# Kernel optimization log

Hardware: AMD Instinct MI355X
Metric: run time of the kernel (lower is better)

Reference implementation:

```python
import jax, jax.numpy as jnp
import numpy as np

B, S, D, E, NH, R, L = 512, 23, 768, 8, 8, 256, 50
TOP_K = 2
LN_EPS = 1e-5  # torch LayerNorm default


def _ln(x, g, b):
    m = jnp.mean(x, axis=-1, keepdims=True)
    v = jnp.mean((x - m) ** 2, axis=-1, keepdims=True)
    return (x - m) * jax.lax.rsqrt(v + LN_EPS) * g + b


def setup_inputs() -> dict:
    key = jax.random.key(0)
    it = iter(jax.random.split(key, 32))
    def p(shape, scale=0.02):
        return jax.random.normal(next(it), shape, dtype=jnp.float32) * scale
    inp = {
        'section_embeddings': jax.random.normal(next(it), (B, S, D), dtype=jnp.float32),
        'existing': jax.random.randint(next(it), (B, S), 0, 2, dtype=jnp.int32),
        'missing_table': p((S, D), 0.05),
        # DeepPositionEncoder per expert (num_layers=3): D->R->R->R->D + LN(D)
        'dpe_w0': p((E, D, R)), 'dpe_b0': jnp.zeros((E, R), jnp.float32),
        'dpe_w1': p((E, R, R)), 'dpe_b1': jnp.zeros((E, R), jnp.float32),
        'dpe_w2': p((E, R, R)), 'dpe_b2': jnp.zeros((E, R), jnp.float32),
        'dpe_wo': p((E, R, D)), 'dpe_bo': jnp.zeros((E, D), jnp.float32),
        'dpe_ln_g': jnp.ones((E, D), jnp.float32), 'dpe_ln_b': jnp.zeros((E, D), jnp.float32),
        # fusion_mlp: cat([context,pos]) (2D)->R->D ; W1 split into context/pos halves
        'fus_w1c': p((E, D, R)), 'fus_w1p': p((E, D, R)), 'fus_b1': jnp.zeros((E, R), jnp.float32),
        'fus_w2': p((E, R, D)), 'fus_b2': jnp.zeros((E, D), jnp.float32),
        # gate_mlp: 2D->R->1, sigmoid
        'gate_w1c': p((E, D, R)), 'gate_w1p': p((E, D, R)), 'gate_b1': jnp.zeros((E, R), jnp.float32),
        'gate_w2': p((E, R, 1)), 'gate_b2': jnp.zeros((E, 1), jnp.float32),
        'exp_ln_g': jnp.ones((E, D), jnp.float32), 'exp_ln_b': jnp.zeros((E, D), jnp.float32),
        # router: 2D->R->E
        'rtr_w1': p((2 * D, R)), 'rtr_b1': jnp.zeros((R,), jnp.float32),
        'rtr_w2': p((R, E)), 'rtr_b2': jnp.zeros((E,), jnp.float32),
        # SectionDimReducer: D->D//2->R + LN(R)
        'red_w1': p((D, D // 2)), 'red_b1': jnp.zeros((D // 2,), jnp.float32),
        'red_w2': p((D // 2, R)), 'red_b2': jnp.zeros((R,), jnp.float32),
        'red_ln_g': jnp.ones((R,), jnp.float32), 'red_ln_b': jnp.zeros((R,), jnp.float32),
        # MultiheadAttention (embed_dim=R, heads=NH)
        'qkv_w': p((3, R, R)), 'qkv_b': jnp.zeros((3, R), jnp.float32),
        'out_w': p((R, R)), 'out_b': jnp.zeros((R,), jnp.float32),
        # predictor
        'pred_w': p((R, L)), 'pred_b': jnp.zeros((L,), jnp.float32),
    }
    return inp


def reference(section_embeddings, existing, missing_table,
              dpe_w0, dpe_b0, dpe_w1, dpe_b1, dpe_w2, dpe_b2, dpe_wo, dpe_bo,
              dpe_ln_g, dpe_ln_b,
              fus_w1c, fus_w1p, fus_b1, fus_w2, fus_b2,
              gate_w1c, gate_w1p, gate_b1, gate_w2, gate_b2,
              exp_ln_g, exp_ln_b,
              rtr_w1, rtr_b1, rtr_w2, rtr_b2,
              red_w1, red_b1, red_w2, red_b2, red_ln_g, red_ln_b,
              qkv_w, qkv_b, out_w, out_b, pred_w, pred_b):
    mask = existing.astype(section_embeddings.dtype)[..., None]         # [B,S,1]
    # masked mean context over present sections
    context = (section_embeddings * mask).sum(1) / (mask.sum(1) + 1e-8)  # [B,D]
    T = B * S
    default = jnp.broadcast_to(missing_table[None], (B, S, D)).reshape(T, D)
    ctx = jnp.broadcast_to(context[:, None, :], (B, S, D)).reshape(T, D)
    # --- all experts, dense (as in source) ---
    h = jax.nn.relu(jnp.einsum('td,edh->teh', default, dpe_w0) + dpe_b0)
    h = jax.nn.relu(jnp.einsum('teh,ehk->tek', h, dpe_w1) + dpe_b1)
    h = jax.nn.relu(jnp.einsum('teh,ehk->tek', h, dpe_w2) + dpe_b2)
    pos = _ln(jnp.einsum('teh,ehd->ted', h, dpe_wo) + dpe_bo + default[:, None, :],
              dpe_ln_g, dpe_ln_b)                                        # [T,E,D]
    hf = jax.nn.relu(jnp.einsum('td,edh->teh', ctx, fus_w1c)
                     + jnp.einsum('ted,edh->teh', pos, fus_w1p) + fus_b1)
    cand = jnp.einsum('teh,ehd->ted', hf, fus_w2) + fus_b2
    hg = jax.nn.relu(jnp.einsum('td,edh->teh', ctx, gate_w1c)
                     + jnp.einsum('ted,edh->teh', pos, gate_w1p) + gate_b1)
    gate = jax.nn.sigmoid(jnp.einsum('teh,eho->teo', hg, gate_w2) + gate_b2)  # [T,E,1]
    exp_out = _ln(gate * cand + (1.0 - gate) * ctx[:, None, :], exp_ln_g, exp_ln_b)  # [T,E,D]
    # --- router: softmax -> top-k -> sparse scatter ---
    rin = jnp.concatenate([default, ctx], axis=-1)                      # [T,2D]
    scores = jax.nn.relu(rin @ rtr_w1 + rtr_b1) @ rtr_w2 + rtr_b2       # [T,E]
    w = jax.nn.softmax(scores, axis=-1)
    tv, ti = jax.lax.top_k(w, TOP_K)
    sw = jnp.zeros_like(w).at[jnp.arange(T)[:, None], ti].set(tv)       # [T,E]
    imputed = jnp.einsum('ted,te->td', exp_out, sw).reshape(B, S, D)
    sec = mask * section_embeddings + (1.0 - mask) * imputed            # [B,S,D]
    # --- reducer ---
    x = jax.nn.gelu(sec @ red_w1 + red_b1, approximate=False)
    x = jax.nn.gelu(x @ red_w2 + red_b2, approximate=False)
    x = _ln(x, red_ln_g, red_ln_b)                                      # [B,S,R]
    # --- MHA self-attention over sections ---
    hd = R // NH
    q = (x @ qkv_w[0] + qkv_b[0]).reshape(B, S, NH, hd)
    k = (x @ qkv_w[1] + qkv_b[1]).reshape(B, S, NH, hd)
    v = (x @ qkv_w[2] + qkv_b[2]).reshape(B, S, NH, hd)
    att = jax.nn.softmax(jnp.einsum('bqhd,bkhd->bhqk', q, k) / np.sqrt(hd), axis=-1)
    o = jnp.einsum('bhqk,bkhd->bqhd', att, v).reshape(B, S, R)
    o = o @ out_w + out_b
    logits = o.mean(axis=1) @ pred_w + pred_b                           # [B,L]
    return logits
```

## Files before the change

kernel.cpp:

```cpp
#include <hip/hip_runtime.h>
#include <hip/hip_bf16.h>
#include <math.h>

#define BB  512
#define SS  23
#define DD  768
#define EE  8
#define NHH 8
#define RR  256
#define HDD 32
#define LL  50
#define HH2 384
#define TT  (BB*SS)
#define LN_EPS 1e-5f
#define MAXWORK 1536
#define NCTX 4352
#define NACAP 12288

typedef short v8s __attribute__((ext_vector_type(8)));
typedef float v4f __attribute__((ext_vector_type(4)));

__device__ __forceinline__ float gelu(float v){
  return 0.5f*v*(1.f + erff(v*0.70710678118654752f));
}
__device__ __forceinline__ unsigned short f2b(float v){
  __hip_bfloat16 h = __float2bfloat16(v);
  return *reinterpret_cast<unsigned short*>(&h);
}

__device__ __forceinline__ float block_sum(float v, float* red, int nw){
  #pragma unroll
  for (int o = 32; o > 0; o >>= 1) v += __shfl_down(v, o, 64);
  int wid = threadIdx.x >> 6;
  __syncthreads();
  if ((threadIdx.x & 63) == 0) red[wid] = v;
  __syncthreads();
  float s = 0.f;
  for (int i = 0; i < nw; ++i) s += red[i];
  return s;
}

__global__ void k_context(const float* __restrict__ emb, const int* __restrict__ existing,
                          float* __restrict__ ctx, unsigned short* __restrict__ ctxbf){
  int b = blockIdx.x, tid = threadIdx.x;
  float acc0=0.f, acc1=0.f, acc2=0.f;
  int cnt = 0;
  for (int s = 0; s < SS; ++s){
    if (existing[b*SS + s]){
      ++cnt;
      const float* row = emb + ((size_t)(b*SS + s))*DD;
      acc0 += row[tid]; acc1 += row[tid+256]; acc2 += row[tid+512];
    }
  }
  float inv = 1.0f / ((float)cnt + 1e-8f);
  float v0 = acc0*inv, v1 = acc1*inv, v2 = acc2*inv;
  ctx[(size_t)b*DD + tid      ] = v0;
  ctx[(size_t)b*DD + tid + 256] = v1;
  ctx[(size_t)b*DD + tid + 512] = v2;
  ctxbf[(size_t)b*DD + tid      ] = f2b(v0);
  ctxbf[(size_t)b*DD + tid + 256] = f2b(v1);
  ctxbf[(size_t)b*DD + tid + 512] = f2b(v2);
}

__global__ void k_mtpad(const float* __restrict__ mt, unsigned short* __restrict__ mtbf){
  int row = blockIdx.x, tid = threadIdx.x;
  #pragma unroll
  for (int j = 0; j < 3; ++j){
    int d = tid + j*256;
    float v = (row < SS) ? mt[(size_t)row*DD + d] : 0.f;
    mtbf[(size_t)row*DD + d] = f2b(v);
  }
}

__global__ __launch_bounds__(256) void k_pack(
    const float* __restrict__ red_w1, const float* __restrict__ qkv_w,
    const float* __restrict__ out_w,  const float* __restrict__ fus_w1c,
    const float* __restrict__ gate_w1c, const float* __restrict__ fus_w2,
    const float* __restrict__ rtr_w1,
    const float* __restrict__ dpe_w0, const float* __restrict__ dpe_w1,
    const float* __restrict__ dpe_w2, const float* __restrict__ dpe_wo,
    const float* __restrict__ fus_w1p, const float* __restrict__ gate_w1p,
    unsigned short* __restrict__ Wr1t, unsigned short* __restrict__ Wqt,
    unsigned short* __restrict__ Wot,  unsigned short* __restrict__ Wct,
    unsigned short* __restrict__ Wf2t,
    unsigned short* __restrict__ W0t,  unsigned short* __restrict__ W1t,
    unsigned short* __restrict__ W2t,  unsigned short* __restrict__ Wot2,
    unsigned short* __restrict__ Wpgt, unsigned short* __restrict__ Wr1rt){
  int t = blockIdx.x, tid = threadIdx.x;
  const float* src; unsigned short* dst;
  int Nsrc, stride, tk, tn;
  if (t < 288){ src = red_w1; dst = Wr1t; Nsrc = 384; stride = 768; tk = t % 24; tn = t / 24; }
  else if (t < 480){
    int u = t - 288, m = u >> 6, v2 = u & 63;
    src = qkv_w + (size_t)m*256*256; dst = Wqt + (size_t)m*256*256;
    Nsrc = 256; stride = 256; tk = v2 & 7; tn = v2 >> 3;
  } else if (t < 544){
    int v2 = t - 480;
    src = out_w; dst = Wot; Nsrc = 256; stride = 256; tk = v2 & 7; tn = v2 >> 3;
  } else if (t < 2080){
    int u = t - 544, e = u / 192, v2 = u % 192;
    src = fus_w1c + (size_t)e*DD*RR; dst = Wct + (size_t)(e*256)*768;
    Nsrc = 256; stride = 768; tk = v2 % 24; tn = v2 / 24;
  } else if (t < 3616){
    int u = t - 2080, e = u / 192, v2 = u % 192;
    src = gate_w1c + (size_t)e*DD*RR; dst = Wct + (size_t)(2048 + e*256)*768;
    Nsrc = 256; stride = 768; tk = v2 % 24; tn = v2 / 24;
  } else if (t < 5152){
    int u = t - 3616, e = u / 192, v2 = u % 192;
    src = fus_w2 + (size_t)e*RR*DD; dst = Wf2t + (size_t)e*768*256;
    Nsrc = 768; stride = 256; tk = v2 & 7; tn = v2 >> 3;
  } else if (t < 5344){
    int u = t - 5152;
    src = rtr_w1 + (size_t)768*256; dst = Wct + (size_t)4096*768;
    Nsrc = 256; stride = 768; tk = u % 24; tn = u / 24;
  } else if (t < 6880){
    int u = t - 5344, e = u / 192, v2 = u % 192;
    src = dpe_w0 + (size_t)e*DD*RR; dst = W0t + (size_t)e*256*768;
    Nsrc = 256; stride = 768; tk = v2 % 24; tn = v2 / 24;
  } else if (t < 7392){
    int u = t - 6880, e = u / 64, v2 = u % 64;
    src = dpe_w1 + (size_t)e*RR*RR; dst = W1t + (size_t)e*256*256;
    Nsrc = 256; stride = 256; tk = v2 & 7; tn = v2 >> 3;
  } else if (t < 7904){
    int u = t - 7392, e = u / 64, v2 = u % 64;
    src = dpe_w2 + (size_t)e*RR*RR; dst = W2t + (size_t)e*256*256;
    Nsrc = 256; stride = 256; tk = v2 & 7; tn = v2 >> 3;
  } else if (t < 9440){
    int u = t - 7904, e = u / 192, v2 = u % 192;
    src = dpe_wo + (size_t)e*RR*DD; dst = Wot2 + (size_t)e*768*256;
    Nsrc = 768; stride = 256; tk = v2 & 7; tn = v2 >> 3;
  } else if (t < 10976){
    int u = t - 9440, e = u / 192, v2 = u % 192;
    src = fus_w1p + (size_t)e*DD*RR; dst = Wpgt + (size_t)e*512*768;
    Nsrc = 256; stride = 768; tk = v2 % 24; tn = v2 / 24;
  } else if (t < 12512){
    int u = t - 10976, e = u / 192, v2 = u % 192;
    src = gate_w1p + (size_t)e*DD*RR; dst = Wpgt + (size_t)e*512*768 + (size_t)256*768;
    Nsrc = 256; stride = 768; tk = v2 % 24; tn = v2 / 24;
  } else {
    int u = t - 12512;
    src = rtr_w1; dst = Wr1rt;
    Nsrc = 256; stride = 768; tk = u % 24; tn = u / 24;
  }
  __shared__ float lt[32][33];
  int i0 = tid >> 5, j = tid & 31;
  #pragma unroll
  for (int l = 0; l < 4; ++l){
    int i = i0 + l*8;
    lt[i][j] = src[(size_t)(tk*32 + i)*Nsrc + tn*32 + j];
  }
  __syncthreads();
  #pragma unroll
  for (int l = 0; l < 4; ++l){
    int i = i0 + l*8;
    dst[(size_t)(tn*32 + i)*stride + tk*32 + j] = f2b(lt[j][i]);
  }
}

__global__ __launch_bounds__(256) void k_gemm(
    const unsigned short* __restrict__ A, const unsigned short* __restrict__ Bt,
    const float* __restrict__ bias, float* __restrict__ C,
    int M, int N, int K, int epi){
  int m0 = blockIdx.x * 64, n0 = blockIdx.y * 64;
  int tid = threadIdx.x;
  int w = tid >> 6, lane = tid & 63;
  int fm = lane & 15, q = lane >> 4;
  __shared__ unsigned short As[64*72];
  __shared__ unsigned short Bs[64*72];
  v4f acc[4] = {};
  int sr = tid >> 2, scb = (tid & 3) * 16;
  const unsigned short* Aga = A + (size_t)(m0 + sr)*K + scb;
  const unsigned short* Bga = Bt + (size_t)(n0 + sr)*K + scb;
  unsigned short* Asd = As + sr*72 + scb;
  unsigned short* Bsd = Bs + sr*72 + scb;
  for (int k0 = 0; k0 < K; k0 += 64){
    uint4 a0 = *(const uint4*)(Aga + k0);
    uint4 a1 = *(const uint4*)(Aga + k0 + 8);
    uint4 b0 = *(const uint4*)(Bga + k0);
    uint4 b1 = *(const uint4*)(Bga + k0 + 8);
    __syncthreads();
    *(uint4*)Asd = a0; *(uint4*)(Asd + 8) = a1;
    *(uint4*)Bsd = b0; *(uint4*)(Bsd + 8) = b1;
    __syncthreads();
    const unsigned short* ap = As + (w*16 + fm)*72 + q*8;
    const unsigned short* bp = Bs + fm*72 + q*8;
    #pragma unroll
    for (int kk = 0; kk < 2; ++kk){
      v8s af = *(const v8s*)(ap + kk*32);
      #pragma unroll
      for (int j = 0; j < 4; ++j){
        v8s bf = *(const v8s*)(bp + j*16*72 + kk*32);
        acc[j] = __builtin_amdgcn_mfma_f32_16x16x32_bf16(af, bf, acc[j], 0, 0, 0);
      }
    }
  }
  #pragma unroll
  for (int j = 0; j < 4; ++j){
    int n = n0 + j*16 + fm;
    float bv = bias ? bias[n] : 0.f;
    float* Cp = C + (size_t)(m0 + w*16 + q*4)*N + n;
    #pragma unroll
    for (int r = 0; r < 4; ++r){
      float v = acc[j][r] + bv;
      if (epi == 2) v = gelu(v);
      Cp[(size_t)r*N] = v;
    }
  }
}

__global__ __launch_bounds__(256) void k_gemmb(
    const unsigned short* __restrict__ A, size_t sA,
    const unsigned short* __restrict__ Bt, size_t sB,
    const float* __restrict__ bias, int sbias,
    void* __restrict__ C, size_t sC,
    int M, int N, int K, int epi){
  int e = blockIdx.z;
  const unsigned short* Ae = A + (size_t)e*sA;
  const unsigned short* Be = Bt + (size_t)e*sB;
  const float* biase = bias ? (bias + (size_t)e*sbias) : (const float*)nullptr;
  int m0 = blockIdx.x * 64, n0 = blockIdx.y * 64;
  int tid = threadIdx.x;
  int w = tid >> 6, lane = tid & 63;
  int fm = lane & 15, q = lane >> 4;
  __shared__ unsigned short As[64*72];
  __shared__ unsigned short Bs[64*72];
  v4f acc[4] = {};
  int sr = tid >> 2, scb = (tid & 3) * 16;
  const unsigned short* Aga = Ae + (size_t)(m0 + sr)*K + scb;
  const unsigned short* Bga = Be + (size_t)(n0 + sr)*K + scb;
  unsigned short* Asd = As + sr*72 + scb;
  unsigned short* Bsd = Bs + sr*72 + scb;
  for (int k0 = 0; k0 < K; k0 += 64){
    uint4 a0 = *(const uint4*)(Aga + k0);
    uint4 a1 = *(const uint4*)(Aga + k0 + 8);
    uint4 b0 = *(const uint4*)(Bga + k0);
    uint4 b1 = *(const uint4*)(Bga + k0 + 8);
    __syncthreads();
    *(uint4*)Asd = a0; *(uint4*)(Asd + 8) = a1;
    *(uint4*)Bsd = b0; *(uint4*)(Bsd + 8) = b1;
    __syncthreads();
    const unsigned short* ap = As + (w*16 + fm)*72 + q*8;
    const unsigned short* bp = Bs + fm*72 + q*8;
    #pragma unroll
    for (int kk = 0; kk < 2; ++kk){
      v8s af = *(const v8s*)(ap + kk*32);
      #pragma unroll
      for (int j = 0; j < 4; ++j){
        v8s bf = *(const v8s*)(bp + j*16*72 + kk*32);
        acc[j] = __builtin_amdgcn_mfma_f32_16x16x32_bf16(af, bf, acc[j], 0, 0, 0);
      }
    }
  }
  #pragma unroll
  for (int j = 0; j < 4; ++j){
    int n = n0 + j*16 + fm;
    float bv = biase ? biase[n] : 0.f;
    #pragma unroll
    for (int r = 0; r < 4; ++r){
      float v = acc[j][r] + bv;
      int m = m0 + w*16 + q*4 + r;
      if (epi == 0){
        unsigned short* Cb = (unsigned short*)C + (size_t)e*sC;
        Cb[(size_t)m*N + n] = f2b(fmaxf(v, 0.f));
      } else {
        float* Cf = (float*)C + (size_t)e*sC;
        Cf[(size_t)m*N + n] = v;
      }
    }
  }
}

__global__ void k_posLN(const float* __restrict__ dpeout, const float* __restrict__ mt,
                        const float* __restrict__ lng, const float* __restrict__ lnb,
                        unsigned short* __restrict__ posbf){
  int e = blockIdx.x >> 6, s = blockIdx.x & 63, tid = threadIdx.x;
  size_t ro = (size_t)(e*64 + s)*DD;
  if (s >= SS){
    for (int j = tid; j < DD; j += 256) posbf[ro + j] = 0;
    return;
  }
  __shared__ float red[8];
  float o[3];
  #pragma unroll
  for (int j = 0; j < 3; ++j){
    int d = tid + j*256;
    o[j] = dpeout[ro + d] + mt[(size_t)s*DD + d];
  }
  float mean = block_sum(o[0]+o[1]+o[2], red, 4) * (1.f/DD);
  float dv = 0.f;
  #pragma unroll
  for (int j = 0; j < 3; ++j){ float c = o[j]-mean; dv += c*c; }
  float rstd = rsqrtf(block_sum(dv, red, 4) * (1.f/DD) + LN_EPS);
  #pragma unroll
  for (int j = 0; j < 3; ++j){
    int d = tid + j*256;
    posbf[ro + d] = f2b((o[j]-mean)*rstd*lng[e*DD + d] + lnb[e*DD + d]);
  }
}

__global__ __launch_bounds__(256) void k_router(
    const float* __restrict__ emb, const int* __restrict__ existing,
    const float* __restrict__ rtrD, const float* __restrict__ ctxFGR,
    const float* __restrict__ rb1, const float* __restrict__ rw2,
    const float* __restrict__ rb2,
    int* __restrict__ cntE, int* __restrict__ listE,
    int* __restrict__ bp0, int* __restrict__ bp1, float* __restrict__ w01,
    unsigned short* __restrict__ secbf){
  int wv = threadIdx.x >> 6, lane = threadIdx.x & 63;
  int tbase = blockIdx.x * 64;
  __shared__ int   easc[128];
  __shared__ float wasc[128];
  __shared__ int   slotA[128];
  for (int ii = wv*16; ii < wv*16 + 16; ++ii){
    int t = tbase + ii;
    if (existing[t]){
      #pragma unroll
      for (int j = 0; j < DD/64; ++j)
        secbf[(size_t)t*DD + lane + j*64] = f2b(emb[(size_t)t*DD + lane + j*64]);
      if (lane == 0){ easc[2*ii] = -1; easc[2*ii+1] = -1; }
      continue;
    }
    int b = t / SS, s = t - b*SS;
    const float* rtrC = ctxFGR + (size_t)b*NCTX + 4096;
    float acc[EE] = {};
    #pragma unroll
    for (int j = 0; j < 4; ++j){
      int idx = lane + j*64;
      float hr = fmaxf(rtrD[s*RR + idx] + rtrC[idx] + rb1[idx], 0.f);
      #pragma unroll
      for (int e = 0; e < EE; ++e) acc[e] += hr * rw2[idx*EE + e];
    }
    #pragma unroll
    for (int e = 0; e < EE; ++e)
      #pragma unroll
      for (int o = 32; o > 0; o >>= 1) acc[e] += __shfl_xor(acc[e], o, 64);
    if (lane == 0){
      float sc[EE];
      float m = -1e30f;
      #pragma unroll
      for (int e = 0; e < EE; ++e){ sc[e] = acc[e] + rb2[e]; m = fmaxf(m, sc[e]); }
      float w[EE]; float Z = 0.f;
      #pragma unroll
      for (int e = 0; e < EE; ++e){ w[e] = expf(sc[e]-m); Z += w[e]; }
      int i0 = 0;
      for (int e = 1; e < EE; ++e) if (w[e] > w[i0]) i0 = e;
      int i1 = -1;
      for (int e = 0; e < EE; ++e) if (e != i0 && (i1 < 0 || w[e] > w[i1])) i1 = e;
      float iz = 1.f/Z;
      easc[2*ii]   = i0; wasc[2*ii]   = w[i0]*iz;
      easc[2*ii+1] = i1; wasc[2*ii+1] = w[i1]*iz;
    }
  }
  __syncthreads();
  if (threadIdx.x < EE){
    int e = threadIdx.x, c = 0;
    for (int j = 0; j < 128; ++j) if (easc[j] == e) ++c;
    int base = c ? atomicAdd(&cntE[e], c) : 0;
    int sl = base;
    for (int j = 0; j < 128; ++j) if (easc[j] == e) slotA[j] = sl++;
  }
  __syncthreads();
  if (threadIdx.x < 128){
    int j = threadIdx.x, e = easc[j];
    if (e >= 0){
      int t = tbase + (j >> 1);
      int sl = slotA[j];
      if (sl >= TT) sl = TT - 1;
      listE[e*TT + sl] = t;
      int bp = (e << 16) | sl;
      if (j & 1){ bp1[t] = bp; w01[2*t+1] = wasc[j]; }
      else      { bp0[t] = bp; w01[2*t]   = wasc[j]; }
    }
  }
}

__global__ void k_offsE(const int* __restrict__ cntE, int* __restrict__ offE,
                        int* __restrict__ workE, int* __restrict__ wtotE){
  if (threadIdx.x == 0){
    int acc = 0, wb = 0;
    for (int e = 0; e < EE; ++e){
      offE[e] = acc;
      int n = cntE[e]; if (n > TT) n = TT;
      acc += n;
      int nb = (n + 63) >> 6;
      for (int j = 0; j < nb && wb < MAXWORK; ++j) workE[wb++] = (e << 16) | j;
    }
    wtotE[0] = wb;
  }
}

__global__ __launch_bounds__(256) void k_hfE(
    const float* __restrict__ ctxFGR, const float* __restrict__ posFG,
    const float* __restrict__ fb1,
    const float* __restrict__ gb1, const float* __restrict__ gw2,
    const float* __restrict__ gb2,
    const int* __restrict__ cntE, const int* __restrict__ offE,
    const int* __restrict__ listE,
    const int* __restrict__ workE, const int* __restrict__ wtotE,
    unsigned short* __restrict__ hfg, float* __restrict__ gatesg){
  int wi = blockIdx.x;
  if (wi >= wtotE[0]) return;
  int ent = workE[wi];
  int e = ent >> 16, chunk = ent & 0xffff;
  int n = cntE[e]; if (n > TT) n = TT;
  int nt = n - chunk*64; if (nt > 64) nt = 64;
  int base = offE[e] + chunk*64;
  int tid = threadIdx.x, wv = tid >> 6, lane = tid & 63;
  __shared__ int tb[64], ts[64];
  if (tid < 64){
    int ok = tid < nt;
    int t = listE[e*TT + chunk*64 + (ok ? tid : 0)];
    tb[tid] = t/SS; ts[tid] = t - (t/SS)*SS;
  }
  __syncthreads();
  {
    int row = tid >> 2, cb = (tid & 3) * 64;
    if (row < nt){
      int b = tb[row], s = ts[row];
      const float4* cF = (const float4*)(ctxFGR + (size_t)b*NCTX + e*256 + cb);
      const float4* pF = (const float4*)(posFG + ((size_t)(e*64 + s))*512 + cb);
      const float4* bF = (const float4*)(fb1 + (size_t)e*RR + cb);
      uint2* dst = (uint2*)(hfg + (size_t)(base + row)*256 + cb);
      #pragma unroll
      for (int j = 0; j < 16; ++j){
        float4 a = cF[j], p = pF[j], bb = bF[j];
        uint2 pk;
        pk.x = (unsigned)f2b(fmaxf(a.x+p.x+bb.x, 0.f))
             | ((unsigned)f2b(fmaxf(a.y+p.y+bb.y, 0.f)) << 16);
        pk.y = (unsigned)f2b(fmaxf(a.z+p.z+bb.z, 0.f))
             | ((unsigned)f2b(fmaxf(a.w+p.w+bb.w, 0.f)) << 16);
        dst[j] = pk;
      }
    }
  }
  for (int ii = 0; ii < 16; ++ii){
    int row = wv*16 + ii;
    if (row < nt){
      int b = tb[row], s = ts[row];
      float g = 0.f;
      #pragma unroll
      for (int j = 0; j < 4; ++j){
        int idx = lane + j*64;
        float hg = fmaxf(ctxFGR[(size_t)b*NCTX + 2048 + e*256 + idx]
                         + posFG[((size_t)(e*64 + s))*512 + 256 + idx] + gb1[e*RR + idx], 0.f);
        g += hg * gw2[e*RR + idx];
      }
      #pragma unroll
      for (int o = 32; o > 0; o >>= 1) g += __shfl_xor(g, o, 64);
      if (lane == 0) gatesg[base + row] = 1.f/(1.f + expf(-(g + gb2[e])));
    }
  }
}

__global__ __launch_bounds__(256) void k_gemmE(
    const unsigned short* __restrict__ hfg, const unsigned short* __restrict__ Wf2t,
    const float* __restrict__ fb2, const float* __restrict__ ctx,
    const float* __restrict__ gatesg,
    const int* __restrict__ cntE, const int* __restrict__ offE,
    const int* __restrict__ listE,
    const int* __restrict__ workE, const int* __restrict__ wtotE,
    float* __restrict__ cand){
  int wi = blockIdx.x;
  if (wi >= wtotE[0]) return;
  int ent = workE[wi];
  int e = ent >> 16, chunk = ent & 0xffff;
  int n = cntE[e]; if (n > TT) n = TT;
  int nt = n - chunk*64; if (nt > 64) nt = 64;
  int base = offE[e] + chunk*64;
  int nc = blockIdx.y;
  int tid = threadIdx.x, w = tid >> 6, lane = tid & 63;
  int fm = lane & 15, q = lane >> 4;
  __shared__ unsigned short As[64*72];
  __shared__ unsigned short Bs[64*72];
  __shared__ float gl[64];
  __shared__ int tbl[64];
  if (tid < 64){
    int ok = tid < nt;
    int t = listE[e*TT + chunk*64 + (ok ? tid : 0)];
    tbl[tid] = t/SS;
    gl[tid] = gatesg[base + (ok ? tid : 0)];
  }
  v4f acc[4] = {};
  int sr = tid >> 2, scb = (tid & 3) * 16;
  const unsigned short* Aga = hfg + (size_t)(base + sr)*256 + scb;
  const unsigned short* Bga = Wf2t + (size_t)e*768*256 + (size_t)(nc*64 + sr)*256 + scb;
  unsigned short* Asd = As + sr*72 + scb;
  unsigned short* Bsd = Bs + sr*72 + scb;
  for (int k0 = 0; k0 < 256; k0 += 64){
    uint4 a0 = *(const uint4*)(Aga + k0);
    uint4 a1 = *(const uint4*)(Aga + k0 + 8);
    uint4 b0 = *(const uint4*)(Bga + k0);
    uint4 b1 = *(const uint4*)(Bga + k0 + 8);
    __syncthreads();
    *(uint4*)Asd = a0; *(uint4*)(Asd + 8) = a1;
    *(uint4*)Bsd = b0; *(uint4*)(Bsd + 8) = b1;
    __syncthreads();
    const unsigned short* ap = As + (w*16 + fm)*72 + q*8;
    const unsigned short* bp = Bs + fm*72 + q*8;
    #pragma unroll
    for (int kk = 0; kk < 2; ++kk){
      v8s af = *(const v8s*)(ap + kk*32);
      #pragma unroll
      for (int j = 0; j < 4; ++j){
        v8s bf = *(const v8s*)(bp + j*16*72 + kk*32);
        acc[j] = __builtin_amdgcn_mfma_f32_16x16x32_bf16(af, bf, acc[j], 0, 0, 0);
      }
    }
  }
  #pragma unroll
  for (int j = 0; j < 4; ++j){
    int d = nc*64 + j*16 + fm;
    float fb2v = fb2[(size_t)e*DD + d];
    #pragma unroll
    for (int r = 0; r < 4; ++r){
      int row = w*16 + q*4 + r;
      if (row < nt){
        float g = gl[row];
        float cv = ctx[(size_t)tbl[row]*DD + d];
        cand[(size_t)(base + row)*DD + d] = g*(acc[j][r] + fb2v) + (1.f - g)*cv;
      }
    }
  }
}

__global__ void k_gather(const int* __restrict__ existing,
                         const int* __restrict__ bp0, const int* __restrict__ bp1,
                         const float* __restrict__ w01, const int* __restrict__ offE,
                         const float* __restrict__ cand,
                         const float* __restrict__ elng, const float* __restrict__ elnb,
                         unsigned short* __restrict__ secbf){
  int wv = threadIdx.x >> 6, lane = threadIdx.x & 63;
  int t = blockIdx.x*4 + wv;
  if (existing[t]) return;
  int b0v = bp0[t], b1v = bp1[t];
  int e0 = b0v >> 16, e1 = b1v >> 16;
  int g0 = offE[e0] + (b0v & 0xffff);
  int g1 = offE[e1] + (b1v & 0xffff);
  if (g0 >= NACAP) g0 = 0;
  if (g1 >= NACAP) g1 = 0;
  float w0 = w01[2*t], w1 = w01[2*t+1];
  float v0[12], v1[12];
  float s0 = 0.f, q0 = 0.f, s1 = 0.f, q1 = 0.f;
  #pragma unroll
  for (int j = 0; j < 12; ++j){
    int d = lane + j*64;
    v0[j] = cand[(size_t)g0*DD + d];
    v1[j] = cand[(size_t)g1*DD + d];
    s0 += v0[j]; q0 += v0[j]*v0[j];
    s1 += v1[j]; q1 += v1[j]*v1[j];
  }
  #pragma unroll
  for (int o = 32; o > 0; o >>= 1){
    s0 += __shfl_xor(s0, o, 64); q0 += __shfl_xor(q0, o, 64);
    s1 += __shfl_xor(s1, o, 64); q1 += __shfl_xor(q1, o, 64);
  }
  float mean0 = s0*(1.f/DD), mean1 = s1*(1.f/DD);
  float rstd0 = rsqrtf(q0*(1.f/DD) - mean0*mean0 + LN_EPS);
  float rstd1 = rsqrtf(q1*(1.f/DD) - mean1*mean1 + LN_EPS);
  #pragma unroll
  for (int j = 0; j < 12; ++j){
    int d = lane + j*64;
    float o0 = (v0[j]-mean0)*rstd0*elng[e0*DD + d] + elnb[e0*DD + d];
    float o1 = (v1[j]-mean1)*rstd1*elng[e1*DD + d] + elnb[e1*DD + d];
    secbf[(size_t)t*DD + d] = f2b(w0*o0 + w1*o1);
  }
}

__global__ __launch_bounds__(256) void k_red2(
    const float* __restrict__ x1, const float* __restrict__ w2, const float* __restrict__ b2v,
    const float* __restrict__ lng, const float* __restrict__ lnb,
    unsigned short* __restrict__ xrbf){
  int t0 = blockIdx.x * 16, tid = threadIdx.x;
  int ty = tid >> 6, tx = tid & 63;
  __shared__ float sx[16*HH2];
  {
    const float4* src = (const float4*)(x1 + (size_t)t0*HH2);
    float4* dst = (float4*)sx;
    for (int i = tid; i < 16*HH2/4; i += 256) dst[i] = src[i];
  }
  __syncthreads();
  float a[4][4] = {};
  const float* W = w2 + tx*4;
  #pragma unroll 8
  for (int d = 0; d < HH2; ++d){
    float4 w = *(const float4*)(W + (size_t)d*RR);
    #pragma unroll
    for (int i = 0; i < 4; ++i){
      float xv = sx[(ty*4+i)*HH2 + d];
      a[i][0]+=xv*w.x; a[i][1]+=xv*w.y; a[i][2]+=xv*w.z; a[i][3]+=xv*w.w;
    }
  }
  float4 bb = *(const float4*)(b2v + tx*4);
  float4 g4 = *(const float4*)(lng + tx*4);
  float4 be4 = *(const float4*)(lnb + tx*4);
  #pragma unroll
  for (int i = 0; i < 4; ++i){
    float v0=gelu(a[i][0]+bb.x), v1=gelu(a[i][1]+bb.y);
    float v2=gelu(a[i][2]+bb.z), v3=gelu(a[i][3]+bb.w);
    float sum = v0+v1+v2+v3;
    float sq  = v0*v0+v1*v1+v2*v2+v3*v3;
    #pragma unroll
    for (int o = 32; o > 0; o >>= 1){ sum += __shfl_xor(sum,o,64); sq += __shfl_xor(sq,o,64); }
    float mean = sum*(1.f/RR);
    float rstd = rsqrtf(sq*(1.f/RR) - mean*mean + LN_EPS);
    float o0 = (v0-mean)*rstd*g4.x + be4.x;
    float o1 = (v1-mean)*rstd*g4.y + be4.y;
    float o2 = (v2-mean)*rstd*g4.z + be4.z;
    float o3 = (v3-mean)*rstd*g4.w + be4.w;
    uint2 pk;
    pk.x = (unsigned)f2b(o0) | ((unsigned)f2b(o1) << 16);
    pk.y = (unsigned)f2b(o2) | ((unsigned)f2b(o3) << 16);
    *(uint2*)(xrbf + (size_t)(t0+ty*4+i)*RR + tx*4) = pk;
  }
}

__global__ void k_attn(const float* __restrict__ qcat, unsigned short* __restrict__ attnbf){
  int bh = blockIdx.x, b = bh / NHH, h = bh % NHH, tid = threadIdx.x;
  __shared__ float qs[SS][HDD], ks[SS][HDD], vs[SS][HDD];
  __shared__ float scr[SS][SS+1];
  for (int idx = tid; idx < SS*HDD; idx += 256){
    int s = idx / HDD, d = idx % HDD;
    size_t g = ((size_t)(b*SS + s))*768 + h*HDD + d;
    qs[s][d] = qcat[g]; ks[s][d] = qcat[g + 256]; vs[s][d] = qcat[g + 512];
  }
  __syncthreads();
  const float scale = 0.17677669529663687f;
  for (int idx = tid; idx < SS*SS; idx += 256){
    int qi = idx / SS, ki = idx % SS;
    float a = 0.f;
    #pragma unroll
    for (int d = 0; d < HDD; ++d) a += qs[qi][d]*ks[ki][d];
    scr[qi][ki] = a*scale;
  }
  __syncthreads();
  if (tid < SS){
    float m = -1e30f;
    for (int ki = 0; ki < SS; ++ki) m = fmaxf(m, scr[tid][ki]);
    float Z = 0.f;
    for (int ki = 0; ki < SS; ++ki){ float e2 = expf(scr[tid][ki]-m); scr[tid][ki] = e2; Z += e2; }
    float iz = 1.f/Z;
    for (int ki = 0; ki < SS; ++ki) scr[tid][ki] *= iz;
  }
  __syncthreads();
  for (int idx = tid; idx < SS*HDD; idx += 256){
    int qi = idx / HDD, d = idx % HDD;
    float a = 0.f;
    for (int ki = 0; ki < SS; ++ki) a += scr[qi][ki]*vs[ki][d];
    attnbf[((size_t)(b*SS + qi))*RR + h*HDD + d] = f2b(a);
  }
}

__global__ void k_final(const float* __restrict__ oproj, const float* __restrict__ pw,
                        const float* __restrict__ pb, float* __restrict__ out){
  int b = blockIdx.x, tid = threadIdx.x;
  __shared__ float om[RR];
  float a = 0.f;
  for (int s = 0; s < SS; ++s) a += oproj[((size_t)(b*SS + s))*RR + tid];
  om[tid] = a * (1.f/SS);
  __syncthreads();
  if (tid < LL){
    float acc = pb[tid];
    for (int h = 0; h < RR; ++h) acc += om[h]*pw[h*LL + tid];
    out[b*LL + tid] = acc;
  }
}

extern "C" void kernel_launch(void* const* d_in, const int* in_sizes, int n_in,
                              void* d_out, int out_size, void* d_ws, size_t ws_size,
                              hipStream_t stream){
  (void)in_sizes; (void)n_in; (void)out_size; (void)ws_size;
  const float* emb      = (const float*)d_in[0];
  const int*   existing = (const int*)d_in[1];
  const float* mt       = (const float*)d_in[2];
  const float* dpe_w0   = (const float*)d_in[3];
  const float* dpe_b0   = (const float*)d_in[4];
  const float* dpe_w1   = (const float*)d_in[5];
  const float* dpe_b1   = (const float*)d_in[6];
  const float* dpe_w2   = (const float*)d_in[7];
  const float* dpe_b2   = (const float*)d_in[8];
  const float* dpe_wo   = (const float*)d_in[9];
  const float* dpe_bo   = (const float*)d_in[10];
  const float* dpe_lng  = (const float*)d_in[11];
  const float* dpe_lnb  = (const float*)d_in[12];
  const float* fus_w1c  = (const float*)d_in[13];
  const float* fus_w1p  = (const float*)d_in[14];
  const float* fus_b1   = (const float*)d_in[15];
  const float* fus_w2   = (const float*)d_in[16];
  const float* fus_b2   = (const float*)d_in[17];
  const float* gate_w1c = (const float*)d_in[18];
  const float* gate_w1p = (const float*)d_in[19];
  const float* gate_b1  = (const float*)d_in[20];
  const float* gate_w2  = (const float*)d_in[21];
  const float* gate_b2  = (const float*)d_in[22];
  const float* exp_lng  = (const float*)d_in[23];
  const float* exp_lnb  = (const float*)d_in[24];
  const float* rtr_w1   = (const float*)d_in[25];
  const float* rtr_b1   = (const float*)d_in[26];
  const float* rtr_w2   = (const float*)d_in[27];
  const float* rtr_b2   = (const float*)d_in[28];
  const float* red_w1   = (const float*)d_in[29];
  const float* red_b1   = (const float*)d_in[30];
  const float* red_w2   = (const float*)d_in[31];
  const float* red_b2   = (const float*)d_in[32];
  const float* red_lng  = (const float*)d_in[33];
  const float* red_lnb  = (const float*)d_in[34];
  const float* qkv_w    = (const float*)d_in[35];
  const float* qkv_b    = (const float*)d_in[36];
  const float* out_w    = (const float*)d_in[37];
  const float* out_b    = (const float*)d_in[38];
  const float* pred_w   = (const float*)d_in[39];
  const float* pred_b   = (const float*)d_in[40];
  float* out = (float*)d_out;

  float* wsf = (float*)d_ws;
  size_t off = 0;
  float* ctx    = wsf + off; off += (size_t)BB*DD;
  unsigned short* ctxbf = (unsigned short*)(wsf + off); off += (size_t)BB*DD/2;
  float* ctxFGR = wsf + off; off += (size_t)BB*NCTX;
  int*   cntE   = (int*)(wsf + off); off += 64;
  int*   workE  = (int*)(wsf + off); off += MAXWORK;
  int*   wtot   = (int*)(wsf + off); off += 64;
  int*   offE   = wtot + 8;
  float* regA   = wsf + off; off += (size_t)128*TT;
  int*   listE  = (int*)regA;
  int*   bp0    = (int*)regA + (size_t)EE*TT;
  int*   bp1    = (int*)regA + (size_t)(EE+1)*TT;
  float* w01    = regA + (size_t)(EE+2)*TT;
  unsigned short* attnbf = (unsigned short*)regA;
  float* regB   = wsf + off; off += (size_t)TT*DD/2;
  unsigned short* secbf = (unsigned short*)regB;
  float* oprojf = regB;
  float* regC   = wsf + off; off += (size_t)NACAP*DD;
  float* dpeout = regC;
  unsigned short* posbf = (unsigned short*)(regC + 393216);
  unsigned short* h0    = (unsigned short*)(regC + 589824);
  unsigned short* h1    = (unsigned short*)(regC + 655360);
  unsigned short* h2    = (unsigned short*)(regC + 720896);
  float* cand   = regC;
  float* x1     = regC;
  float* qcat   = regC;
  float* regD   = wsf + off; off += (size_t)NACAP*256/2;
  unsigned short* hfg  = (unsigned short*)regD;
  unsigned short* xrbf = (unsigned short*)regD;
  unsigned short* Wr1t = (unsigned short*)(wsf + off); off += (size_t)768*384/2;
  unsigned short* Wqt  = (unsigned short*)(wsf + off); off += (size_t)768*256/2;
  unsigned short* Wot  = (unsigned short*)(wsf + off); off += (size_t)256*256/2;
  unsigned short* Wct  = (unsigned short*)(wsf + off); off += (size_t)NCTX*768/2;
  unsigned short* Wf2t = (unsigned short*)(wsf + off); off += (size_t)EE*768*256/2;
  unsigned short* mtbf = (unsigned short*)(wsf + off); off += (size_t)64*768/2;
  unsigned short* W0t  = (unsigned short*)(wsf + off); off += (size_t)EE*256*768/2;
  unsigned short* W1t  = (unsigned short*)(wsf + off); off += (size_t)EE*256*256/2;
  unsigned short* W2t  = (unsigned short*)(wsf + off); off += (size_t)EE*256*256/2;
  unsigned short* Wot2 = (unsigned short*)(wsf + off); off += (size_t)EE*768*256/2;
  unsigned short* Wpgt = (unsigned short*)(wsf + off); off += (size_t)EE*512*768/2;
  unsigned short* Wr1rt= (unsigned short*)(wsf + off); off += (size_t)256*768/2;
  float* posFG  = wsf + off; off += (size_t)EE*64*512;
  float* rtrDp  = wsf + off; off += (size_t)64*256;
  float* gatesg = wsf + off; off += (size_t)NACAP;

  k_context<<<BB, 256, 0, stream>>>(emb, existing, ctx, ctxbf);
  k_mtpad  <<<64, 256, 0, stream>>>(mt, mtbf);
  k_pack   <<<12704, 256, 0, stream>>>(red_w1, qkv_w, out_w, fus_w1c, gate_w1c, fus_w2,
                                       rtr_w1, dpe_w0, dpe_w1, dpe_w2, dpe_wo,
                                       fus_w1p, gate_w1p,
                                       Wr1t, Wqt, Wot, Wct, Wf2t,
                                       W0t, W1t, W2t, Wot2, Wpgt, Wr1rt);
  k_gemmb<<<dim3(1,4,8),  256, 0, stream>>>(mtbf, 0, W0t, (size_t)256*768,
                                            dpe_b0, 256, h0, (size_t)64*256,
                                            64, 256, 768, 0);
  k_gemmb<<<dim3(1,4,8),  256, 0, stream>>>(h0, (size_t)64*256, W1t, (size_t)256*256,
                                            dpe_b1, 256, h1, (size_t)64*256,
                                            64, 256, 256, 0);
  k_gemmb<<<dim3(1,4,8),  256, 0, stream>>>(h1, (size_t)64*256, W2t, (size_t)256*256,
                                            dpe_b2, 256, h2, (size_t)64*256,
                                            64, 256, 256, 0);
  k_gemmb<<<dim3(1,12,8), 256, 0, stream>>>(h2, (size_t)64*256, Wot2, (size_t)768*256,
                                            dpe_bo, 768, dpeout, (size_t)64*768,
                                            64, 768, 256, 1);
  k_posLN<<<512, 256, 0, stream>>>(dpeout, mt, dpe_lng, dpe_lnb, posbf);
  k_gemmb<<<dim3(1,8,8),  256, 0, stream>>>(posbf, (size_t)64*768, Wpgt, (size_t)512*768,
                                            (const float*)nullptr, 0, posFG, (size_t)64*512,
                                            64, 512, 768, 1);
  k_gemmb<<<dim3(1,4,1),  256, 0, stream>>>(mtbf, 0, Wr1rt, 0,
                                            (const float*)nullptr, 0, rtrDp, 0,
                                            64, 256, 768, 1);
  {
    dim3 g(BB/64, NCTX/64);
    k_gemm <<<g, 256, 0, stream>>>(ctxbf, Wct, (const float*)nullptr, ctxFGR,
                                   BB, NCTX, DD, 0);
  }
  hipMemsetAsync(cntE, 0, 64*sizeof(int), stream);
  k_router <<<TT/64, 256, 0, stream>>>(emb, existing, rtrDp, ctxFGR, rtr_b1, rtr_w2, rtr_b2,
                                       cntE, listE, bp0, bp1, w01, secbf);
  k_offsE  <<<1, 64, 0, stream>>>(cntE, offE, workE, wtot);
  k_hfE    <<<384, 256, 0, stream>>>(ctxFGR, posFG, fus_b1,
                                     gate_b1, gate_w2, gate_b2,
                                     cntE, offE, listE, workE, wtot, hfg, gatesg);
  k_gemmE  <<<dim3(384,12), 256, 0, stream>>>(hfg, Wf2t, fus_b2, ctx, gatesg,
                                              cntE, offE, listE, workE, wtot, cand);
  k_gather <<<TT/4, 256, 0, stream>>>(existing, bp0, bp1, w01, offE, cand,
                                      exp_lng, exp_lnb, secbf);
  {
    dim3 g(TT/64, HH2/64);
    k_gemm <<<g, 256, 0, stream>>>(secbf, Wr1t, red_b1, x1, TT, HH2, DD, 2);
  }
  k_red2   <<<TT/16, 256, 0, stream>>>(x1, red_w2, red_b2, red_lng, red_lnb, xrbf);
  {
    dim3 g(TT/64, 768/64);
    k_gemm <<<g, 256, 0, stream>>>(xrbf, Wqt, qkv_b, qcat, TT, 768, RR, 1);
  }
  k_attn   <<<BB*NHH, 256, 0, stream>>>(qcat, attnbf);
  {
    dim3 g(TT/64, RR/64);
    k_gemm <<<g, 256, 0, stream>>>(attnbf, Wot, out_b, oprojf, TT, RR, RR, 1);
  }
  k_final  <<<BB, 256, 0, stream>>>(oprojf, pred_w, pred_b, out);
}
```

Baseline: 515.0 us.

## Move reducer second layer to bf16 MFMA GEMM and simplify router slot allocation

The scalar fp32 k_red2 kernel is replaced with a bf16 MFMA GEMM. The first reducer GEMM now writes GELU output as bf16, red_w2 is packed and transposed, and a separate warp-per-token LayerNorm kernel follows. The router kernel is also restructured to one wavefront per token with per-token atomics in place of block-level shared-memory slot aggregation, and it copies existing rows with vectorized conversion. Together these aim to cut the FP32 FMA cost of the reducer and the serial per-block router work, at the price of an extra launch, more global atomics, and bf16 rounding of the intermediate activations.

```diff
diff --git a/kernel.cpp b/kernel.cpp
--- a/kernel.cpp
+++ b/kernel.cpp
@@ -80,12 +80,14 @@
     const float* __restrict__ dpe_w0, const float* __restrict__ dpe_w1,
     const float* __restrict__ dpe_w2, const float* __restrict__ dpe_wo,
     const float* __restrict__ fus_w1p, const float* __restrict__ gate_w1p,
+    const float* __restrict__ red_w2,
     unsigned short* __restrict__ Wr1t, unsigned short* __restrict__ Wqt,
     unsigned short* __restrict__ Wot,  unsigned short* __restrict__ Wct,
     unsigned short* __restrict__ Wf2t,
     unsigned short* __restrict__ W0t,  unsigned short* __restrict__ W1t,
     unsigned short* __restrict__ W2t,  unsigned short* __restrict__ Wot2,
-    unsigned short* __restrict__ Wpgt, unsigned short* __restrict__ Wr1rt){
+    unsigned short* __restrict__ Wpgt, unsigned short* __restrict__ Wr1rt,
+    unsigned short* __restrict__ Wr2t){
   int t = blockIdx.x, tid = threadIdx.x;
   const float* src; unsigned short* dst;
   int Nsrc, stride, tk, tn;
@@ -137,10 +139,14 @@
     int u = t - 10976, e = u / 192, v2 = u % 192;
     src = gate_w1p + (size_t)e*DD*RR; dst = Wpgt + (size_t)e*512*768 + (size_t)256*768;
     Nsrc = 256; stride = 768; tk = v2 % 24; tn = v2 / 24;
-  } else {
+  } else if (t < 12704){
     int u = t - 12512;
     src = rtr_w1; dst = Wr1rt;
     Nsrc = 256; stride = 768; tk = u % 24; tn = u / 24;
+  } else {
+    int u = t - 12704;
+    src = red_w2; dst = Wr2t;
+    Nsrc = 256; stride = 384; tk = u % 12; tn = u / 12;
   }
   __shared__ float lt[32][33];
   int i0 = tid >> 5, j = tid & 31;
@@ -198,12 +204,19 @@
   for (int j = 0; j < 4; ++j){
     int n = n0 + j*16 + fm;
     float bv = bias ? bias[n] : 0.f;
-    float* Cp = C + (size_t)(m0 + w*16 + q*4)*N + n;
-    #pragma unroll
-    for (int r = 0; r < 4; ++r){
-      float v = acc[j][r] + bv;
-      if (epi == 2) v = gelu(v);
-      Cp[(size_t)r*N] = v;
+    if (epi == 3){
+      unsigned short* Cp = (unsigned short*)C + (size_t)(m0 + w*16 + q*4)*N + n;
+      #pragma unroll
+      for (int r = 0; r < 4; ++r)
+        Cp[(size_t)r*N] = f2b(gelu(acc[j][r] + bv));
+    } else {
+      float* Cp = C + (size_t)(m0 + w*16 + q*4)*N + n;
+      #pragma unroll
+      for (int r = 0; r < 4; ++r){
+        float v = acc[j][r] + bv;
+        if (epi == 2) v = gelu(v);
+        Cp[(size_t)r*N] = v;
+      }
     }
   }
 }
@@ -307,70 +320,55 @@
     int* __restrict__ bp0, int* __restrict__ bp1, float* __restrict__ w01,
     unsigned short* __restrict__ secbf){
   int wv = threadIdx.x >> 6, lane = threadIdx.x & 63;
-  int tbase = blockIdx.x * 64;
-  __shared__ int   easc[128];
-  __shared__ float wasc[128];
-  __shared__ int   slotA[128];
-  for (int ii = wv*16; ii < wv*16 + 16; ++ii){
-    int t = tbase + ii;
-    if (existing[t]){
-      #pragma unroll
-      for (int j = 0; j < DD/64; ++j)
-        secbf[(size_t)t*DD + lane + j*64] = f2b(emb[(size_t)t*DD + lane + j*64]);
-      if (lane == 0){ easc[2*ii] = -1; easc[2*ii+1] = -1; }
-      continue;
-    }
-    int b = t / SS, s = t - b*SS;
-    const float* rtrC = ctxFGR + (size_t)b*NCTX + 4096;
-    float acc[EE] = {};
-    #pragma unroll
-    for (int j = 0; j < 4; ++j){
-      int idx = lane + j*64;
-      float hr = fmaxf(rtrD[s*RR + idx] + rtrC[idx] + rb1[idx], 0.f);
-      #pragma unroll
-      for (int e = 0; e < EE; ++e) acc[e] += hr * rw2[idx*EE + e];
-    }
-    #pragma unroll
-    for (int e = 0; e < EE; ++e)
-      #pragma unroll
-      for (int o = 32; o > 0; o >>= 1) acc[e] += __shfl_xor(acc[e], o, 64);
-    if (lane == 0){
-      float sc[EE];
-      float m = -1e30f;
-      #pragma unroll
-      for (int e = 0; e < EE; ++e){ sc[e] = acc[e] + rb2[e]; m = fmaxf(m, sc[e]); }
-      float w[EE]; float Z = 0.f;
-      #pragma unroll
-      for (int e = 0; e < EE; ++e){ w[e] = expf(sc[e]-m); Z += w[e]; }
-      int i0 = 0;
-      for (int e = 1; e < EE; ++e) if (w[e] > w[i0]) i0 = e;
-      int i1 = -1;
-      for (int e = 0; e < EE; ++e) if (e != i0 && (i1 < 0 || w[e] > w[i1])) i1 = e;
-      float iz = 1.f/Z;
-      easc[2*ii]   = i0; wasc[2*ii]   = w[i0]*iz;
-      easc[2*ii+1] = i1; wasc[2*ii+1] = w[i1]*iz;
-    }
-  }
-  __syncthreads();
-  if (threadIdx.x < EE){
-    int e = threadIdx.x, c = 0;
-    for (int j = 0; j < 128; ++j) if (easc[j] == e) ++c;
-    int base = c ? atomicAdd(&cntE[e], c) : 0;
-    int sl = base;
-    for (int j = 0; j < 128; ++j) if (easc[j] == e) slotA[j] = sl++;
-  }
-  __syncthreads();
-  if (threadIdx.x < 128){
-    int j = threadIdx.x, e = easc[j];
-    if (e >= 0){
-      int t = tbase + (j >> 1);
-      int sl = slotA[j];
-      if (sl >= TT) sl = TT - 1;
-      listE[e*TT + sl] = t;
-      int bp = (e << 16) | sl;
-      if (j & 1){ bp1[t] = bp; w01[2*t+1] = wasc[j]; }
-      else      { bp0[t] = bp; w01[2*t]   = wasc[j]; }
-    }
+  int t = blockIdx.x*4 + wv;
+  if (existing[t]){
+    const float4* src = (const float4*)(emb + (size_t)t*DD);
+    uint2* dst = (uint2*)(secbf + (size_t)t*DD);
+    #pragma unroll
+    for (int j = 0; j < 3; ++j){
+      float4 x = src[lane + j*64];
+      uint2 pk;
+      pk.x = (unsigned)f2b(x.x) | ((unsigned)f2b(x.y) << 16);
+      pk.y = (unsigned)f2b(x.z) | ((unsigned)f2b(x.w) << 16);
+      dst[lane + j*64] = pk;
+    }
+    return;
+  }
+  int b = t / SS, s = t - b*SS;
+  const float* rtrC = ctxFGR + (size_t)b*NCTX + 4096;
+  float acc[EE] = {};
+  #pragma unroll
+  for (int j = 0; j < 4; ++j){
+    int idx = lane + j*64;
+    float hr = fmaxf(rtrD[s*RR + idx] + rtrC[idx] + rb1[idx], 0.f);
+    #pragma unroll
+    for (int e = 0; e < EE; ++e) acc[e] += hr * rw2[idx*EE + e];
+  }
+  #pragma unroll
+  for (int e = 0; e < EE; ++e)
+    #pragma unroll
+    for (int o = 32; o > 0; o >>= 1) acc[e] += __shfl_xor(acc[e], o, 64);
+  if (lane == 0){
+    float sc[EE];
+    float m = -1e30f;
+    #pragma unroll
+    for (int e = 0; e < EE; ++e){ sc[e] = acc[e] + rb2[e]; m = fmaxf(m, sc[e]); }
+    float w[EE]; float Z = 0.f;
+    #pragma unroll
+    for (int e = 0; e < EE; ++e){ w[e] = expf(sc[e]-m); Z += w[e]; }
+    int i0 = 0;
+    for (int e = 1; e < EE; ++e) if (w[e] > w[i0]) i0 = e;
+    int i1 = -1;
+    for (int e = 0; e < EE; ++e) if (e != i0 && (i1 < 0 || w[e] > w[i1])) i1 = e;
+    float iz = 1.f/Z;
+    int sl0 = atomicAdd(&cntE[i0], 1);
+    int sl1 = atomicAdd(&cntE[i1], 1);
+    if (sl0 >= TT) sl0 = TT - 1;
+    if (sl1 >= TT) sl1 = TT - 1;
+    listE[i0*TT + sl0] = t;
+    listE[i1*TT + sl1] = t;
+    bp0[t] = (i0 << 16) | sl0; w01[2*t]   = w[i0]*iz;
+    bp1[t] = (i1 << 16) | sl1; w01[2*t+1] = w[i1]*iz;
   }
 }
 
@@ -566,51 +564,28 @@
   }
 }
 
-__global__ __launch_bounds__(256) void k_red2(
-    const float* __restrict__ x1, const float* __restrict__ w2, const float* __restrict__ b2v,
-    const float* __restrict__ lng, const float* __restrict__ lnb,
-    unsigned short* __restrict__ xrbf){
-  int t0 = blockIdx.x * 16, tid = threadIdx.x;
-  int ty = tid >> 6, tx = tid & 63;
-  __shared__ float sx[16*HH2];
-  {
-    const float4* src = (const float4*)(x1 + (size_t)t0*HH2);
-    float4* dst = (float4*)sx;
-    for (int i = tid; i < 16*HH2/4; i += 256) dst[i] = src[i];
-  }
-  __syncthreads();
-  float a[4][4] = {};
-  const float* W = w2 + tx*4;
-  #pragma unroll 8
-  for (int d = 0; d < HH2; ++d){
-    float4 w = *(const float4*)(W + (size_t)d*RR);
-    #pragma unroll
-    for (int i = 0; i < 4; ++i){
-      float xv = sx[(ty*4+i)*HH2 + d];
-      a[i][0]+=xv*w.x; a[i][1]+=xv*w.y; a[i][2]+=xv*w.z; a[i][3]+=xv*w.w;
-    }
-  }
-  float4 bb = *(const float4*)(b2v + tx*4);
-  float4 g4 = *(const float4*)(lng + tx*4);
-  float4 be4 = *(const float4*)(lnb + tx*4);
-  #pragma unroll
-  for (int i = 0; i < 4; ++i){
-    float v0=gelu(a[i][0]+bb.x), v1=gelu(a[i][1]+bb.y);
-    float v2=gelu(a[i][2]+bb.z), v3=gelu(a[i][3]+bb.w);
-    float sum = v0+v1+v2+v3;
-    float sq  = v0*v0+v1*v1+v2*v2+v3*v3;
-    #pragma unroll
-    for (int o = 32; o > 0; o >>= 1){ sum += __shfl_xor(sum,o,64); sq += __shfl_xor(sq,o,64); }
-    float mean = sum*(1.f/RR);
-    float rstd = rsqrtf(sq*(1.f/RR) - mean*mean + LN_EPS);
-    float o0 = (v0-mean)*rstd*g4.x + be4.x;
-    float o1 = (v1-mean)*rstd*g4.y + be4.y;
-    float o2 = (v2-mean)*rstd*g4.z + be4.z;
-    float o3 = (v3-mean)*rstd*g4.w + be4.w;
-    uint2 pk;
-    pk.x = (unsigned)f2b(o0) | ((unsigned)f2b(o1) << 16);
-    pk.y = (unsigned)f2b(o2) | ((unsigned)f2b(o3) << 16);
-    *(uint2*)(xrbf + (size_t)(t0+ty*4+i)*RR + tx*4) = pk;
+__global__ void k_lnR(const float* __restrict__ x2f,
+                      const float* __restrict__ lng, const float* __restrict__ lnb,
+                      unsigned short* __restrict__ xrbf){
+  int wv = threadIdx.x >> 6, lane = threadIdx.x & 63;
+  int t = blockIdx.x*4 + wv;
+  float v[4];
+  float s = 0.f, q = 0.f;
+  #pragma unroll
+  for (int j = 0; j < 4; ++j){
+    v[j] = x2f[(size_t)t*RR + lane + j*64];
+    s += v[j]; q += v[j]*v[j];
+  }
+  #pragma unroll
+  for (int o = 32; o > 0; o >>= 1){
+    s += __shfl_xor(s, o, 64); q += __shfl_xor(q, o, 64);
+  }
+  float mean = s*(1.f/RR);
+  float rstd = rsqrtf(q*(1.f/RR) - mean*mean + LN_EPS);
+  #pragma unroll
+  for (int j = 0; j < 4; ++j){
+    int d = lane + j*64;
+    xrbf[(size_t)t*RR + d] = f2b((v[j]-mean)*rstd*lng[d] + lnb[d]);
   }
 }
 
@@ -737,7 +712,8 @@
   unsigned short* h1    = (unsigned short*)(regC + 655360);
   unsigned short* h2    = (unsigned short*)(regC + 720896);
   float* cand   = regC;
-  float* x1     = regC;
+  unsigned short* x1bf = (unsigned short*)regC;
+  float* x2f    = regC + 4718592;
   float* qcat   = regC;
   float* regD   = wsf + off; off += (size_t)NACAP*256/2;
   unsigned short* hfg  = (unsigned short*)regD;
@@ -754,17 +730,18 @@
   unsigned short* Wot2 = (unsigned short*)(wsf + off); off += (size_t)EE*768*256/2;
   unsigned short* Wpgt = (unsigned short*)(wsf + off); off += (size_t)EE*512*768/2;
   unsigned short* Wr1rt= (unsigned short*)(wsf + off); off += (size_t)256*768/2;
+  unsigned short* Wr2t = (unsigned short*)(wsf + off); off += (size_t)256*384/2;
   float* posFG  = wsf + off; off += (size_t)EE*64*512;
   float* rtrDp  = wsf + off; off += (size_t)64*256;
   float* gatesg = wsf + off; off += (size_t)NACAP;
 
   k_context<<<BB, 256, 0, stream>>>(emb, existing, ctx, ctxbf);
   k_mtpad  <<<64, 256, 0, stream>>>(mt, mtbf);
-  k_pack   <<<12704, 256, 0, stream>>>(red_w1, qkv_w, out_w, fus_w1c, gate_w1c, fus_w2,
+  k_pack   <<<12800, 256, 0, stream>>>(red_w1, qkv_w, out_w, fus_w1c, gate_w1c, fus_w2,
                                        rtr_w1, dpe_w0, dpe_w1, dpe_w2, dpe_wo,
-                                       fus_w1p, gate_w1p,
+                                       fus_w1p, gate_w1p, red_w2,
                                        Wr1t, Wqt, Wot, Wct, Wf2t,
-                                       W0t, W1t, W2t, Wot2, Wpgt, Wr1rt);
+                                       W0t, W1t, W2t, Wot2, Wpgt, Wr1rt, Wr2t);
   k_gemmb<<<dim3(1,4,8),  256, 0, stream>>>(mtbf, 0, W0t, (size_t)256*768,
                                             dpe_b0, 256, h0, (size_t)64*256,
                                             64, 256, 768, 0);
@@ -790,8 +767,8 @@
                                    BB, NCTX, DD, 0);
   }
   hipMemsetAsync(cntE, 0, 64*sizeof(int), stream);
-  k_router <<<TT/64, 256, 0, stream>>>(emb, existing, rtrDp, ctxFGR, rtr_b1, rtr_w2, rtr_b2,
-                                       cntE, listE, bp0, bp1, w01, secbf);
+  k_router <<<TT/4, 256, 0, stream>>>(emb, existing, rtrDp, ctxFGR, rtr_b1, rtr_w2, rtr_b2,
+                                      cntE, listE, bp0, bp1, w01, secbf);
   k_offsE  <<<1, 64, 0, stream>>>(cntE, offE, workE, wtot);
   k_hfE    <<<384, 256, 0, stream>>>(ctxFGR, posFG, fus_b1,
                                      gate_b1, gate_w2, gate_b2,
@@ -802,9 +779,13 @@
                                       exp_lng, exp_lnb, secbf);
   {
     dim3 g(TT/64, HH2/64);
-    k_gemm <<<g, 256, 0, stream>>>(secbf, Wr1t, red_b1, x1, TT, HH2, DD, 2);
-  }
-  k_red2   <<<TT/16, 256, 0, stream>>>(x1, red_w2, red_b2, red_lng, red_lnb, xrbf);
+    k_gemm <<<g, 256, 0, stream>>>(secbf, Wr1t, red_b1, (float*)x1bf, TT, HH2, DD, 3);
+  }
+  {
+    dim3 g(TT/64, RR/64);
+    k_gemm <<<g, 256, 0, stream>>>(x1bf, Wr2t, red_b2, x2f, TT, RR, HH2, 2);
+  }
+  k_lnR    <<<TT/4, 256, 0, stream>>>(x2f, red_lng, red_lnb, xrbf);
   {
     dim3 g(TT/64, 768/64);
     k_gemm <<<g, 256, 0, stream>>>(xrbf, Wqt, qkv_b, qcat, TT, 768, RR, 1);
```

After: 581.6 us. 1.13x slower.
